# Kernel optimization log

Hardware: AMD Instinct MI355X
Metric: run time of the kernel (lower is better)

## Reference

```python
import jax, jax.numpy as jnp
import numpy as np

B, NC, H, W, C = 4, 3, 112, 112, 128
HEADS, WS, SS = 4, 7, 3
HD = C // HEADS
SCALE = HD ** -0.5
NWIN = (H // WS) * (W // WS)
N = WS * WS  # tokens per window per contrast


def _rel_pos_index():
    # standard Swin relative position index over a WSxWS window
    c = np.stack(np.meshgrid(np.arange(WS), np.arange(WS), indexing='ij')).reshape(2, -1)
    r = (c[:, :, None] - c[:, None, :]).transpose(1, 2, 0)
    r[:, :, 0] += WS - 1
    r[:, :, 1] += WS - 1
    r[:, :, 0] *= 2 * WS - 1
    return r.sum(-1)  # (N, N) int

RPI = _rel_pos_index()


def _attn_mask():
    # SW-MSA mask built exactly as in __init__ (shift active since 0 < SS < WS)
    img = np.zeros((H, W))
    sl = (slice(0, -WS), slice(-WS, -SS), slice(-SS, None))
    cnt = 0
    for hh in sl:
        for ww in sl:
            img[hh, ww] = cnt
            cnt += 1
    mw = img.reshape(H // WS, WS, W // WS, WS).transpose(0, 2, 1, 3).reshape(-1, N)
    am = mw[:, None, :] - mw[:, :, None]  # unsqueeze(1) - unsqueeze(2)
    return jnp.asarray(np.where(am != 0, -100.0, 0.0), dtype=np.float32)  # (nW, N, N)

MASK = _attn_mask()


def win_part(x):
    # (B, n, H, W, C) -> (B*nW, n, WS, WS, C)
    b, n = x.shape[0], x.shape[1]
    x = x.reshape(b, n, H // WS, WS, W // WS, WS, C)
    return x.transpose(0, 2, 4, 1, 3, 5, 6).reshape(-1, n, WS, WS, C)


def win_rev(x, b):
    # (B*nW, n, WS, WS, C) -> (B, n, H, W, C)
    n = x.shape[1]
    x = x.reshape(b, H // WS, W // WS, n, WS, WS, C)
    return x.transpose(0, 3, 1, 4, 2, 5, 6).reshape(b, n, H, W, C)


def ln(x, g, bta):
    m = x.mean(-1, keepdims=True)
    v = ((x - m) ** 2).mean(-1, keepdims=True)
    return (x - m) * jax.lax.rsqrt(v + 1e-5) * g + bta


def win_attn(xq, xk, xv, wq, bq, wk, bk, wv, bv, wp, bp, rpb):
    B_, nq = xq.shape[0], xq.shape[1]
    nkv = xk.shape[1]
    Nq, Nkv = nq * N, nkv * N
    q = (xq.reshape(B_, Nq, C) @ wq + bq).reshape(B_, Nq, HEADS, HD).transpose(0, 2, 1, 3) * SCALE
    k = (xk.reshape(B_, Nkv, C) @ wk + bk).reshape(B_, Nkv, HEADS, HD).transpose(0, 2, 1, 3)
    v = (xv.reshape(B_, Nkv, C) @ wv + bv).reshape(B_, Nkv, HEADS, HD).transpose(0, 2, 1, 3)
    attn = jnp.einsum('bhqd,bhkd->bhqk', q, k)
    bias = jnp.tile(rpb[RPI].transpose(2, 0, 1), (1, nq, nkv))  # (HEADS, Nq, Nkv)
    attn = attn + bias[None]
    m = jnp.tile(MASK, (1, nq, nkv))  # (nW, Nq, Nkv)
    attn = attn.reshape(B_ // NWIN, NWIN, HEADS, Nq, Nkv) + m[None, :, None]
    attn = jax.nn.softmax(attn.reshape(B_, HEADS, Nq, Nkv), axis=-1)
    out = jnp.einsum('bhqk,bhkd->bhqd', attn, v).transpose(0, 2, 1, 3).reshape(B_, Nq, C) @ wp + bp
    return out.reshape(B_, nq, WS, WS, C)


def reference(x, x_kv, contrast_token, contrast_embed,
              n1g, n1b, n2g, n2b, n3g, n3b,
              sa_wq, sa_bq, sa_wk, sa_bk, sa_wv, sa_bv, sa_wp, sa_bp, sa_rpb,
              ca_wq, ca_bq, ca_wk, ca_bk, ca_wv, ca_bv, ca_wp, ca_bp, ca_rpb,
              m_w1, m_b1, m_w2, m_b2):
    ct = contrast_token[None, :, None, None, :]
    ce = contrast_embed[None, :, None, None, :]
    # --- shifted-window self-attention ---
    shortcut = x
    h = ln(x, n1g, n1b)
    h = jnp.roll(h, (-SS, -SS), axis=(2, 3))
    xw = win_part(h)
    xwe = xw + ct
    aw = win_attn(xwe, xwe, xw, sa_wq, sa_bq, sa_wk, sa_bk, sa_wv, sa_bv, sa_wp, sa_bp, sa_rpb)
    h = win_rev(aw, B)
    h = jnp.roll(h, (SS, SS), axis=(2, 3))
    x = shortcut + h
    # --- shifted-window cross-attention against x_kv ---
    shortcut = x
    h = ln(x, n2g, n2b)
    hs = jnp.roll(h, (-SS, -SS), axis=(2, 3))
    kvs = jnp.roll(x_kv, (-SS, -SS), axis=(2, 3))
    xw = win_part(hs)
    kw = win_part(kvs)
    aw = win_attn(xw + ct, kw + ce, kw, ca_wq, ca_bq, ca_wk, ca_bk, ca_wv, ca_bv, ca_wp, ca_bp, ca_rpb)
    h = win_rev(aw, B)
    h = jnp.roll(h, (SS, SS), axis=(2, 3))
    x = shortcut + h
    # --- MLP ---
    h = ln(x, n3g, n3b)
    h = jax.nn.gelu(h @ m_w1 + m_b1, approximate=False) @ m_w2 + m_b2
    return x + h


def setup_inputs():
    key = jax.random.key(0)
    ks = jax.random.split(key, 32)
    rn = lambda i, shp, s=1.0: jax.random.normal(ks[i], shp, dtype=jnp.float32) * s
    inp = {
        'x': rn(0, (B, NC, H, W, C)),
        'x_kv': rn(1, (B, NC, H, W, C)),
        'contrast_token': rn(2, (NC, C), 0.02),
        'contrast_embed': rn(3, (NC, C), 0.02),
        'n1g': jnp.ones((C,)), 'n1b': jnp.zeros((C,)),
        'n2g': jnp.ones((C,)), 'n2b': jnp.zeros((C,)),
        'n3g': jnp.ones((C,)), 'n3b': jnp.zeros((C,)),
    }
    i = 4
    for pre in ('sa', 'ca'):
        for nm in ('wq', 'wk', 'wv', 'wp'):
            inp[pre + '_' + nm] = rn(i, (C, C), 0.02)
            inp[pre + '_b' + nm[1]] = jnp.zeros((C,))
            i += 1
        inp[pre + '_rpb'] = rn(i, ((2 * WS - 1) ** 2, HEADS), 0.02)
        i += 1
    inp['m_w1'] = rn(i, (C, 4 * C), 0.02)
    inp['m_b1'] = jnp.zeros((4 * C,))
    inp['m_w2'] = rn(i + 1, (4 * C, C), 0.02)
    inp['m_b2'] = jnp.zeros((C,))
    return inp
```

## Files before the change

### kernel.cpp

```cpp
#include <hip/hip_runtime.h>
#include <hip/hip_bf16.h>

typedef __hip_bfloat16 bf16;

#define Bn    4
#define NCn   3
#define Hn    112
#define Wn    112
#define Cn    128
#define HEADS 4
#define WSn   7
#define SSn   3
#define HDn   32
#define WNt   1024
#define Tt    147
#define SCALE 0.17677669529663687f

#define SA    288
#define SH    1056
#define MT    32
#define NROWS 49
#define NPAD  64

static const size_t NE = (size_t)Bn * NCn * Hn * Wn * Cn;

typedef float f32x4 __attribute__((ext_vector_type(4)));
typedef short s16x8 __attribute__((ext_vector_type(8)));
typedef short s16x4 __attribute__((ext_vector_type(4)));
#define MFMA(a,b,c) __builtin_amdgcn_mfma_f32_16x16x32_bf16((a),(b),(c),0,0,0)

#define P_QCSA 0
#define P_KCSA 384
#define P_QCCA 768
#define P_KCCA 1152
#define P_VCSA 1536
#define P_BPSA 1664
#define P_VCCA 1792
#define P_BPCA 1920
#define P_B1   2048
#define P_B2   2560
#define P_G1   2688
#define P_N1B  2816
#define P_G2   2944
#define P_N2B  3072
#define P_G3   3200
#define P_N3B  3328

#define W_SAQ 0
#define W_SAK 16384
#define W_SAV 32768
#define W_SAP 49152
#define W_CAQ 65536
#define W_CAK 81920
#define W_CAV 98304
#define W_CAP 114688
#define W_W1T 131072
#define W_W2T 196608

struct Ptrs { const void* p[32]; };

__device__ __forceinline__ float bf2f(bf16 v) { return __bfloat162float(v); }
__device__ __forceinline__ bf16  f2bf(float v) { return __float2bfloat16(v); }
__device__ __forceinline__ short f2bs(float v) { bf16 t = __float2bfloat16(v); return *reinterpret_cast<short*>(&t); }
__device__ __forceinline__ float bs2f(short v) { bf16 t = *reinterpret_cast<bf16*>(&v); return __bfloat162float(t); }

__device__ __forceinline__ float ldi(const void* __restrict__ p, size_t i, int f) {
    return f ? ((const float*)p)[i] : bf2f(((const bf16*)p)[i]);
}

__device__ __forceinline__ float gelu(float x) {
    float x2 = x * x;
    float arg = x * fmaf(x2, 0.0713548162f, 1.5957691216f);
    float e = __expf(arg);
    float r = __builtin_amdgcn_rcpf(1.f + e);
    return x - x * r;
}

__device__ __forceinline__ void ln_inplace(char* __restrict__ rp, const float* __restrict__ gb) {
    float s = 0.f, s2 = 0.f;
    #pragma unroll
    for (int c8 = 0; c8 < 16; ++c8) {
        s16x8 v = *(const s16x8*)(rp + c8 * 16);
        #pragma unroll
        for (int j = 0; j < 8; ++j) { float fv = bs2f(v[j]); s += fv; s2 += fv * fv; }
    }
    float mean = s * (1.f / 128.f);
    float rstd = rsqrtf(s2 * (1.f / 128.f) - mean * mean + 1e-5f);
    #pragma unroll
    for (int c8 = 0; c8 < 16; ++c8) {
        s16x8 v = *(const s16x8*)(rp + c8 * 16);
        #pragma unroll
        for (int j = 0; j < 8; ++j) {
            int col = c8 * 8 + j;
            v[j] = f2bs((bs2f(v[j]) - mean) * rstd * gb[col] + gb[128 + col]);
        }
        *(s16x8*)(rp + c8 * 16) = v;
    }
}

__device__ __forceinline__ void ln_row4(char* __restrict__ rowbase, const float* __restrict__ gb, int sub) {
    char* rp = rowbase + sub * 64;
    float s = 0.f, s2 = 0.f;
    s16x8 vv[4];
    #pragma unroll
    for (int c = 0; c < 4; ++c) {
        vv[c] = *(const s16x8*)(rp + c * 16);
        #pragma unroll
        for (int j = 0; j < 8; ++j) { float fv = bs2f(vv[c][j]); s += fv; s2 += fv * fv; }
    }
    s  += __shfl_xor(s, 1);  s  += __shfl_xor(s, 2);
    s2 += __shfl_xor(s2, 1); s2 += __shfl_xor(s2, 2);
    float mean = s * (1.f / 128.f);
    float rstd = rsqrtf(s2 * (1.f / 128.f) - mean * mean + 1e-5f);
    #pragma unroll
    for (int c = 0; c < 4; ++c) {
        #pragma unroll
        for (int j = 0; j < 8; ++j) {
            int col = sub * 32 + c * 8 + j;
            vv[c][j] = f2bs((bs2f(vv[c][j]) - mean) * rstd * gb[col] + gb[128 + col]);
        }
        *(s16x8*)(rp + c * 16) = vv[c];
    }
}

__device__ __forceinline__ int tok_row(int wn, int t) {
    int b = wn >> 8, wrem = wn & 255, wi = wrem >> 4, wj = wrem & 15;
    int n = t / 49, p = t % 49, pi = p / 7, pj = p % 7;
    int i = (wi * 7 + pi + SSn) % Hn;
    int j = (wj * 7 + pj + SSn) % Wn;
    return ((b * NCn + n) * Hn + i) * Wn + j;
}

__global__ void k_detect(const unsigned int* __restrict__ xw, int* __restrict__ flag) {
    __shared__ int cnt;
    if (threadIdx.x == 0) cnt = 0;
    __syncthreads();
    int c = 0;
    for (int i = threadIdx.x; i < 8192; i += 256) {
        unsigned e = (xw[i] >> 7) & 0xffu;
        c += (e >= 100u && e <= 140u) ? 1 : 0;
    }
    atomicAdd(&cnt, c);
    __syncthreads();
    if (threadIdx.x == 0) *flag = (cnt < 4096) ? 1 : 0;
}

__global__ __launch_bounds__(256) void k_prep(Ptrs in, const int* __restrict__ dflag,
                                              float* __restrict__ P, bf16* __restrict__ wT,
                                              float* __restrict__ BMT) {
    const int f = *dflag;
    int b = blockIdx.x, tid = threadIdx.x;
    if (b == 0) {
        for (int t = tid; t < 384; t += 256) {
            int n = t >> 7, c = t & 127;
            float aq = 0.f, ak = 0.f, aq2 = 0.f, ak2 = 0.f;
            for (int d = 0; d < Cn; ++d) {
                float ctv = ldi(in.p[2], n * Cn + d, f);
                float cev = ldi(in.p[3], n * Cn + d, f);
                aq  += ctv * ldi(in.p[10], d * Cn + c, f);
                ak  += ctv * ldi(in.p[12], d * Cn + c, f);
                aq2 += ctv * ldi(in.p[19], d * Cn + c, f);
                ak2 += cev * ldi(in.p[21], d * Cn + c, f);
            }
            P[P_QCSA + t] = aq  + ldi(in.p[11], c, f);
            P[P_KCSA + t] = ak  + ldi(in.p[13], c, f);
            P[P_QCCA + t] = aq2 + ldi(in.p[20], c, f);
            P[P_KCCA + t] = ak2 + ldi(in.p[22], c, f);
        }
    } else if (b == 1) {
        if (tid < 128) {
            P[P_VCSA + tid] = ldi(in.p[15], tid, f);
            P[P_BPSA + tid] = ldi(in.p[17], tid, f);
            P[P_VCCA + tid] = ldi(in.p[24], tid, f);
            P[P_BPCA + tid] = ldi(in.p[26], tid, f);
            P[P_B2   + tid] = ldi(in.p[31], tid, f);
            P[P_G1   + tid] = ldi(in.p[4],  tid, f);
            P[P_N1B  + tid] = ldi(in.p[5],  tid, f);
            P[P_G2   + tid] = ldi(in.p[6],  tid, f);
            P[P_N2B  + tid] = ldi(in.p[7],  tid, f);
            P[P_G3   + tid] = ldi(in.p[8],  tid, f);
            P[P_N3B  + tid] = ldi(in.p[9],  tid, f);
        }
        for (int t = tid; t < 512; t += 256) P[P_B1 + t] = ldi(in.p[29], t, f);
    } else if (b < 66) {
        const int map[8] = {10, 12, 14, 16, 19, 21, 23, 25};
        int unit = (b - 2) * 4 + (tid >> 6), lane = tid & 63;
        int mat = unit >> 5, ntks = unit & 31;
        int ntile = ntks >> 2, ks = ntks & 3;
        int n = ntile * 16 + (lane & 15), k0 = ks * 32 + (lane >> 4) * 8;
        const void* src = in.p[map[mat]];
        s16x8 v;
        #pragma unroll
        for (int j = 0; j < 8; ++j) v[j] = f2bs(ldi(src, (size_t)(k0 + j) * 128 + n, f));
        *(s16x8*)(wT + mat * 16384 + ((size_t)ntks * 64 + lane) * 8) = v;
    } else if (b < 130) {
        int unit = (b - 66) * 4 + (tid >> 6), lane = tid & 63;
        s16x8 v;
        if (unit < 128) {
            int ntile = unit >> 2, ks = unit & 3;
            int n = ntile * 16 + (lane & 15), k0 = ks * 32 + (lane >> 4) * 8;
            #pragma unroll
            for (int j = 0; j < 8; ++j) v[j] = f2bs(ldi(in.p[28], (size_t)(k0 + j) * 512 + n, f));
            *(s16x8*)(wT + W_W1T + ((size_t)unit * 64 + lane) * 8) = v;
        } else {
            int b2 = unit - 128;
            int ntile = b2 >> 4, ks = b2 & 15;
            int n = ntile * 16 + (lane & 15), k0 = ks * 32 + (lane >> 4) * 8;
            #pragma unroll
            for (int j = 0; j < 8; ++j) v[j] = f2bs(ldi(in.p[30], (size_t)(k0 + j) * 128 + n, f));
            *(s16x8*)(wT + W_W2T + ((size_t)b2 * 64 + lane) * 8) = v;
        }
    } else {
        int u = b - 130;
        int stage = u >> 4, pat = (u >> 2) & 3, h = u & 3;
        const void* rpb = in.p[stage ? 27 : 18];
        float* dst = BMT + (size_t)u * 2560;
        int er = pat >> 1, ec = pat & 1;
        for (int i = tid; i < 2560; i += 256) {
            float v = 0.f;
            int qp = i / 52, kp = i - qp * 52;
            if (qp < 49 && kp < 49) {
                int qpi = qp / 7, qpj = qp - qpi * 7, kpi = kp / 7, kpj = kp - kpi * 7;
                float bias = ldi(rpb, ((qpi - kpi + 6) * 13 + (qpj - kpj + 6)) * HEADS + h, f);
                int rq = (er ? (qpi < 4 ? 1 : 2) : 0) * 3 + (ec ? (qpj < 4 ? 1 : 2) : 0);
                int rk = (er ? (kpi < 4 ? 1 : 2) : 0) * 3 + (ec ? (kpj < 4 ? 1 : 2) : 0);
                v = bias + (rq == rk ? 0.f : -100.f);
            }
            dst[i] = v;
        }
    }
}

__global__ __launch_bounds__(256) void k_qkv_sa(
    const void* __restrict__ x, bf16* __restrict__ xr,
    const float* __restrict__ P, const bf16* __restrict__ wT,
    const int* __restrict__ dflag,
    bf16* __restrict__ tokQ, bf16* __restrict__ tokK, bf16* __restrict__ tokV) {
    const int f = *dflag;
    __shared__ char ldsA[NPAD * SA];
    __shared__ int rowIdx[NROWS];
    __shared__ float gb[256];
    int wn = blockIdx.x, nc = blockIdx.y, tid = threadIdx.x;
    int t0 = nc * NROWS;
    if (tid < NROWS) rowIdx[tid] = tok_row(wn, t0 + tid);
    gb[tid] = tid < 128 ? P[P_G1 + tid] : P[P_N1B + tid - 128];
    for (int i = tid; i < 15 * SA / 4; i += 256) ((int*)(ldsA + NROWS * SA))[i] = 0;
    __syncthreads();
    for (int idx = tid; idx < NROWS * 16; idx += 256) {
        int t = idx >> 4, c8 = idx & 15;
        size_t g = (size_t)rowIdx[t] * Cn + c8 * 8;
        s16x8 v;
        if (f) {
            const float* s = (const float*)x + g;
            #pragma unroll
            for (int j = 0; j < 8; ++j) v[j] = f2bs(s[j]);
        } else {
            v = *(const s16x8*)((const bf16*)x + g);
        }
        *(s16x8*)(ldsA + t * SA + c8 * 16) = v;
        *(s16x8*)(xr + g) = v;
    }
    __syncthreads();
    if (tid < NROWS) ln_inplace(ldsA + tid * SA, gb);
    __syncthreads();
    int wv = tid >> 6, lane = tid & 63, l15 = lane & 15, lg = lane >> 4;
    #pragma unroll 1
    for (int mat = 0; mat < 3; ++mat) {
        const bf16* W = wT + mat * 16384;
        bf16* dst = mat == 0 ? tokQ : (mat == 1 ? tokK : tokV);
        #pragma unroll 1
        for (int ni = 0; ni < 2; ++ni) {
            int nt = wv * 2 + ni;
            f32x4 acc[4] = {};
            #pragma unroll
            for (int ks = 0; ks < 4; ++ks) {
                s16x8 bfrag = *(const s16x8*)(W + (((nt << 2) + ks) * 64 + lane) * 8);
                #pragma unroll
                for (int mt = 0; mt < 4; ++mt) {
                    s16x8 af = *(const s16x8*)(ldsA + (mt * 16 + l15) * SA + ks * 64 + lg * 16);
                    acc[mt] = MFMA(bfrag, af, acc[mt]);
                }
            }
            int col0 = nt * 16 + lg * 4;
            #pragma unroll
            for (int mt = 0; mt < 4; ++mt) {
                int tl = mt * 16 + l15;
                if (tl < NROWS) {
                    int t = t0 + tl;
                    s16x4 pk;
                    if (mat == 0) {
                        f32x4 b4 = *(const f32x4*)(P + P_QCSA + nc * 128 + col0);
                        #pragma unroll
                        for (int r = 0; r < 4; ++r) pk[r] = f2bs((acc[mt][r] + b4[r]) * SCALE);
                    } else if (mat == 1) {
                        f32x4 b4 = *(const f32x4*)(P + P_KCSA + nc * 128 + col0);
                        #pragma unroll
                        for (int r = 0; r < 4; ++r) pk[r] = f2bs(acc[mt][r] + b4[r]);
                    } else {
                        f32x4 b4 = *(const f32x4*)(P + P_VCSA + col0);
                        #pragma unroll
                        for (int r = 0; r < 4; ++r) pk[r] = f2bs(acc[mt][r] + b4[r]);
                    }
                    *(s16x4*)(dst + ((size_t)wn * Tt + t) * Cn + col0) = pk;
                }
            }
        }
    }
}

__global__ __launch_bounds__(512) void k_attn(
    const bf16* __restrict__ Q, const bf16* __restrict__ K, const bf16* __restrict__ V,
    bf16* __restrict__ O, const float* __restrict__ BMbase) {
    __shared__ char ldsK[40 * 256];
    __shared__ char ldsV[32 * 336];
    __shared__ char ldsP[8 * 16 * 336];
    __shared__ float BM[2560];
    __shared__ float lArr[8][16];
    int wn = blockIdx.x, h = blockIdx.y, tid = threadIdx.x;
    int wi = (wn >> 4) & 15, wj = wn & 15;
    size_t base = (size_t)wn * Tt * Cn + h * HDn;
    for (int idx = tid; idx < 640; idx += 512) {
        int key = idx >> 2, ch = idx & 3;
        s16x8 kv = {}, vv = {};
        if (key < Tt) {
            kv = *(const s16x8*)(K + base + (size_t)key * Cn + ch * 8);
            vv = *(const s16x8*)(V + base + (size_t)key * Cn + ch * 8);
        }
        *(s16x8*)(ldsK + (key >> 2) * 256 + (key & 3) * 64 + ch * 16) = kv;
        #pragma unroll
        for (int j = 0; j < 8; ++j)
            *(short*)(ldsV + (ch * 8 + j) * 336 + key * 2) = vv[j];
    }
    {
        int pat = ((wi == 15) << 1) | (wj == 15);
        const f32x4* src = (const f32x4*)(BMbase + (size_t)(pat * 4 + h) * 2560);
        f32x4* dst4 = (f32x4*)BM;
        for (int i = tid; i < 640; i += 512) dst4[i] = src[i];
    }
    __syncthreads();
    int wv = tid >> 6, lane = tid & 63, l15 = lane & 15, lg = lane >> 4;
    char* myP = ldsP + wv * (16 * 336);
    int kpA[10];
    #pragma unroll
    for (int nt = 0; nt < 10; ++nt) {
        int key = nt * 16 + l15;
        kpA[nt] = key - (key >= 147 ? 147 : (key >= 98 ? 98 : (key >= 49 ? 49 : 0)));
    }
    for (int mt = wv; mt < 10; mt += 8) {
        int qrow = mt * 16 + l15; if (qrow > 146) qrow = 146;
        s16x8 qf = *(const s16x8*)(Q + base + (size_t)qrow * Cn + lg * 8);
        f32x4 acc[10];
        #pragma unroll
        for (int nt = 0; nt < 10; ++nt) {
            int key = nt * 16 + l15;
            s16x8 bfrag = *(const s16x8*)(ldsK + (key >> 2) * 256 + (key & 3) * 64 + lg * 16);
            f32x4 z = {};
            acc[nt] = MFMA(qf, bfrag, z);
        }
        float linv[4];
        #pragma unroll
        for (int r = 0; r < 4; ++r) {
            int row = mt * 16 + lg * 4 + r;
            int qp = row - (row >= 147 ? 147 : (row >= 98 ? 98 : (row >= 49 ? 49 : 0)));
            float s[10], m = -1e30f;
            #pragma unroll
            for (int nt = 0; nt < 10; ++nt) {
                float sv = acc[nt][r] + BM[qp * 52 + kpA[nt]];
                if (nt == 9 && l15 >= 3) sv = -1e30f;
                s[nt] = sv;
                m = fmaxf(m, sv);
            }
            #pragma unroll
            for (int off = 1; off < 16; off <<= 1) m = fmaxf(m, __shfl_xor(m, off));
            float l = 0.f;
            #pragma unroll
            for (int nt = 0; nt < 10; ++nt) {
                float p = (nt == 9 && l15 >= 3) ? 0.f : __expf(s[nt] - m);
                l += p;
                *(bf16*)(myP + (lg * 4 + r) * 336 + (nt * 16 + l15) * 2) = f2bf(p);
            }
            #pragma unroll
            for (int off = 1; off < 16; off <<= 1) l += __shfl_xor(l, off);
            linv[r] = 1.f / l;
        }
        if (l15 == 0) {
            #pragma unroll
            for (int r = 0; r < 4; ++r) lArr[wv][lg * 4 + r] = linv[r];
        }
        float myinv = lArr[wv][l15];
        #pragma unroll
        for (int ntv = 0; ntv < 2; ++ntv) {
            f32x4 ao = {};
            #pragma unroll
            for (int ks = 0; ks < 5; ++ks) {
                s16x8 af = *(const s16x8*)(myP + l15 * 336 + ks * 64 + lg * 16);
                s16x8 vf = *(const s16x8*)(ldsV + (ntv * 16 + l15) * 336 + ks * 64 + lg * 16);
                ao = MFMA(vf, af, ao);
            }
            int q = mt * 16 + l15;
            if (q < Tt) {
                s16x4 pk;
                #pragma unroll
                for (int r = 0; r < 4; ++r) pk[r] = f2bs(ao[r] * myinv);
                *(s16x4*)(O + base + (size_t)q * Cn + ntv * 16 + lg * 4) = pk;
            }
        }
    }
}

__global__ __launch_bounds__(256) void k_proj(
    const bf16* __restrict__ tokO, const float* __restrict__ P, const bf16* __restrict__ W,
    int bpOff, bf16* __restrict__ xr) {
    __shared__ char ldsA[NPAD * SA];
    __shared__ int rowIdx[NROWS];
    int wn = blockIdx.x, nc = blockIdx.y, tid = threadIdx.x;
    int t0 = nc * NROWS;
    if (tid < NROWS) rowIdx[tid] = tok_row(wn, t0 + tid);
    for (int i = tid; i < 15 * SA / 4; i += 256) ((int*)(ldsA + NROWS * SA))[i] = 0;
    __syncthreads();
    int wv = tid >> 6, lane = tid & 63, l15 = lane & 15, lg = lane >> 4;
    s16x4 xrc[2][4];
    #pragma unroll
    for (int ni = 0; ni < 2; ++ni) {
        int col0 = (wv * 2 + ni) * 16 + lg * 4;
        #pragma unroll
        for (int mt = 0; mt < 4; ++mt) {
            int tl = mt * 16 + l15;
            int rr = rowIdx[tl < NROWS ? tl : 0];
            xrc[ni][mt] = *(const s16x4*)(xr + (size_t)rr * Cn + col0);
        }
    }
    for (int idx = tid; idx < NROWS * 16; idx += 256) {
        int t = idx >> 4, c8 = idx & 15;
        s16x8 v = *(const s16x8*)(tokO + ((size_t)wn * Tt + t0 + t) * Cn + c8 * 8);
        *(s16x8*)(ldsA + t * SA + c8 * 16) = v;
    }
    __syncthreads();
    f32x4 acc2[2][4] = {};
    #pragma unroll
    for (int ni = 0; ni < 2; ++ni) {
        int nt = wv * 2 + ni;
        #pragma unroll
        for (int ks = 0; ks < 4; ++ks) {
            s16x8 bfrag = *(const s16x8*)(W + (((nt << 2) + ks) * 64 + lane) * 8);
            #pragma unroll
            for (int mt = 0; mt < 4; ++mt) {
                s16x8 af = *(const s16x8*)(ldsA + (mt * 16 + l15) * SA + ks * 64 + lg * 16);
                acc2[ni][mt] = MFMA(bfrag, af, acc2[ni][mt]);
            }
        }
    }
    #pragma unroll
    for (int ni = 0; ni < 2; ++ni) {
        int col0 = (wv * 2 + ni) * 16 + lg * 4;
        f32x4 bp4 = *(const f32x4*)(P + bpOff + col0);
        #pragma unroll
        for (int mt = 0; mt < 4; ++mt) {
            int tl = mt * 16 + l15;
            if (tl < NROWS) {
                s16x4 pk;
                #pragma unroll
                for (int r = 0; r < 4; ++r) pk[r] = f2bs(bs2f(xrc[ni][mt][r]) + acc2[ni][mt][r] + bp4[r]);
                *(s16x4*)(xr + (size_t)rowIdx[tl] * Cn + col0) = pk;
            }
        }
    }
}

__global__ __launch_bounds__(256) void k_proj_ca(
    const bf16* __restrict__ tokO, const float* __restrict__ P, const bf16* __restrict__ wT,
    const void* __restrict__ xkv, const int* __restrict__ dflag, bf16* __restrict__ xr,
    bf16* __restrict__ tokQ, bf16* __restrict__ tokK, bf16* __restrict__ tokV) {
    const int f = *dflag;
    __shared__ char ldsA[NPAD * SA];
    __shared__ int rowIdx[NROWS];
    __shared__ float gb[256];
    int wn = blockIdx.x, nc = blockIdx.y, tid = threadIdx.x;
    int t0 = nc * NROWS;
    if (tid < NROWS) rowIdx[tid] = tok_row(wn, t0 + tid);
    gb[tid] = tid < 128 ? P[P_G2 + tid] : P[P_N2B + tid - 128];
    for (int i = tid; i < 15 * SA / 4; i += 256) ((int*)(ldsA + NROWS * SA))[i] = 0;
    __syncthreads();
    for (int idx = tid; idx < NROWS * 16; idx += 256) {
        int t = idx >> 4, c8 = idx & 15;
        s16x8 v = *(const s16x8*)(tokO + ((size_t)wn * Tt + t0 + t) * Cn + c8 * 8);
        *(s16x8*)(ldsA + t * SA + c8 * 16) = v;
    }
    __syncthreads();
    int wv = tid >> 6, lane = tid & 63, l15 = lane & 15, lg = lane >> 4;
    {
        const bf16* W = wT + W_SAP;
        #pragma unroll 1
        for (int ni = 0; ni < 2; ++ni) {
            int nt = wv * 2 + ni;
            f32x4 acc[4] = {};
            #pragma unroll
            for (int ks = 0; ks < 4; ++ks) {
                s16x8 bfrag = *(const s16x8*)(W + (((nt << 2) + ks) * 64 + lane) * 8);
                #pragma unroll
                for (int mt = 0; mt < 4; ++mt) {
                    s16x8 af = *(const s16x8*)(ldsA + (mt * 16 + l15) * SA + ks * 64 + lg * 16);
                    acc[mt] = MFMA(bfrag, af, acc[mt]);
                }
            }
            int col0 = nt * 16 + lg * 4;
            f32x4 bp4 = *(const f32x4*)(P + P_BPSA + col0);
            #pragma unroll
            for (int mt = 0; mt < 4; ++mt) {
                int tl = mt * 16 + l15;
                if (tl < NROWS) {
                    size_t o = (size_t)rowIdx[tl] * Cn + col0;
                    s16x4 cur = *(const s16x4*)(xr + o);
                    s16x4 pk;
                    #pragma unroll
                    for (int r = 0; r < 4; ++r) pk[r] = f2bs(bs2f(cur[r]) + acc[mt][r] + bp4[r]);
                    *(s16x4*)(xr + o) = pk;
                }
            }
        }
    }
    __syncthreads();
    for (int idx = tid; idx < NROWS * 16; idx += 256) {
        int t = idx >> 4, c8 = idx & 15;
        s16x8 v = *(const s16x8*)(xr + (size_t)rowIdx[t] * Cn + c8 * 8);
        *(s16x8*)(ldsA + t * SA + c8 * 16) = v;
    }
    __syncthreads();
    if (tid < NROWS) ln_inplace(ldsA + tid * SA, gb);
    __syncthreads();
    {
        const bf16* W = wT + W_CAQ;
        #pragma unroll 1
        for (int ni = 0; ni < 2; ++ni) {
            int nt = wv * 2 + ni;
            f32x4 acc[4] = {};
            #pragma unroll
            for (int ks = 0; ks < 4; ++ks) {
                s16x8 bfrag = *(const s16x8*)(W + (((nt << 2) + ks) * 64 + lane) * 8);
                #pragma unroll
                for (int mt = 0; mt < 4; ++mt) {
                    s16x8 af = *(const s16x8*)(ldsA + (mt * 16 + l15) * SA + ks * 64 + lg * 16);
                    acc[mt] = MFMA(bfrag, af, acc[mt]);
                }
            }
            int col0 = nt * 16 + lg * 4;
            #pragma unroll
            for (int mt = 0; mt < 4; ++mt) {
                int tl = mt * 16 + l15;
                if (tl < NROWS) {
                    int t = t0 + tl;
                    f32x4 b4 = *(const f32x4*)(P + P_QCCA + nc * 128 + col0);
                    s16x4 pk;
                    #pragma unroll
                    for (int r = 0; r < 4; ++r) pk[r] = f2bs((acc[mt][r] + b4[r]) * SCALE);
                    *(s16x4*)(tokQ + ((size_t)wn * Tt + t) * Cn + col0) = pk;
                }
            }
        }
    }
    __syncthreads();
    for (int idx = tid; idx < NROWS * 16; idx += 256) {
        int t = idx >> 4, c8 = idx & 15;
        s16x8 v;
        if (f) {
            const float* s = (const float*)xkv + (size_t)rowIdx[t] * Cn + c8 * 8;
            #pragma unroll
            for (int j = 0; j < 8; ++j) v[j] = f2bs(s[j]);
        } else {
            v = *(const s16x8*)((const bf16*)xkv + (size_t)rowIdx[t] * Cn + c8 * 8);
        }
        *(s16x8*)(ldsA + t * SA + c8 * 16) = v;
    }
    __syncthreads();
    #pragma unroll 1
    for (int mat = 0; mat < 2; ++mat) {
        const bf16* W = wT + (mat == 0 ? W_CAK : W_CAV);
        bf16* dst = mat == 0 ? tokK : tokV;
        #pragma unroll 1
        for (int ni = 0; ni < 2; ++ni) {
            int nt = wv * 2 + ni;
            f32x4 acc[4] = {};
            #pragma unroll
            for (int ks = 0; ks < 4; ++ks) {
                s16x8 bfrag = *(const s16x8*)(W + (((nt << 2) + ks) * 64 + lane) * 8);
                #pragma unroll
                for (int mt = 0; mt < 4; ++mt) {
                    s16x8 af = *(const s16x8*)(ldsA + (mt * 16 + l15) * SA + ks * 64 + lg * 16);
                    acc[mt] = MFMA(bfrag, af, acc[mt]);
                }
            }
            int col0 = nt * 16 + lg * 4;
            #pragma unroll
            for (int mt = 0; mt < 4; ++mt) {
                int tl = mt * 16 + l15;
                if (tl < NROWS) {
                    int t = t0 + tl;
                    f32x4 b4 = (mat == 0) ? *(const f32x4*)(P + P_KCCA + nc * 128 + col0)
                                          : *(const f32x4*)(P + P_VCCA + col0);
                    s16x4 pk;
                    #pragma unroll
                    for (int r = 0; r < 4; ++r) pk[r] = f2bs(acc[mt][r] + b4[r]);
                    *(s16x4*)(dst + ((size_t)wn * Tt + t) * Cn + col0) = pk;
                }
            }
        }
    }
}

__global__ __launch_bounds__(256) void k_mlp(
    const bf16* __restrict__ xr, const float* __restrict__ P, const bf16* __restrict__ wT,
    const int* __restrict__ dflag, void* __restrict__ outp) {
    __shared__ char ldsU[MT * SH];
    __shared__ float gb[256];
    char* ldsA = ldsU;
    char* ldsH = ldsU;
    int tid = threadIdx.x;
    size_t t0 = (size_t)blockIdx.x * MT;
    gb[tid] = tid < 128 ? P[P_G3 + tid] : P[P_N3B + tid - 128];
    __syncthreads();
    for (int idx = tid; idx < MT * 16; idx += 256) {
        int t = idx >> 4, c8 = idx & 15;
        s16x8 v = *(const s16x8*)(xr + (t0 + t) * Cn + c8 * 8);
        *(s16x8*)(ldsA + t * SA + c8 * 16) = v;
    }
    __syncthreads();
    {
        int row = tid >> 3, sub = tid & 7;
        if (sub < 4) ln_row4(ldsA + row * SA, gb, sub);
    }
    __syncthreads();
    int wv = tid >> 6, lane = tid & 63, l15 = lane & 15, lg = lane >> 4;
    const bf16* W1 = wT + W_W1T;
    s16x8 a[2][4];
    #pragma unroll
    for (int m = 0; m < 2; ++m)
        #pragma unroll
        for (int ks = 0; ks < 4; ++ks)
            a[m][ks] = *(const s16x8*)(ldsA + (m * 16 + l15) * SA + ks * 64 + lg * 16);
    __syncthreads();
    {
        int nt0 = wv * 8;
        s16x8 bc0 = *(const s16x8*)(W1 + (((nt0 << 2) + 0) * 64 + lane) * 8);
        s16x8 bc1 = *(const s16x8*)(W1 + (((nt0 << 2) + 1) * 64 + lane) * 8);
        s16x8 bc2 = *(const s16x8*)(W1 + (((nt0 << 2) + 2) * 64 + lane) * 8);
        s16x8 bc3 = *(const s16x8*)(W1 + (((nt0 << 2) + 3) * 64 + lane) * 8);
        #pragma unroll 1
        for (int ni = 0; ni < 8; ++ni) {
            int nt = nt0 + ni;
            s16x8 bn0 = *(const s16x8*)(W1 + ((((nt + 1) << 2) + 0) * 64 + lane) * 8);
            s16x8 bn1 = *(const s16x8*)(W1 + ((((nt + 1) << 2) + 1) * 64 + lane) * 8);
            s16x8 bn2 = *(const s16x8*)(W1 + ((((nt + 1) << 2) + 2) * 64 + lane) * 8);
            s16x8 bn3 = *(const s16x8*)(W1 + ((((nt + 1) << 2) + 3) * 64 + lane) * 8);
            f32x4 acc[2] = {};
            #pragma unroll
            for (int m = 0; m < 2; ++m) {
                acc[m] = MFMA(bc0, a[m][0], acc[m]);
                acc[m] = MFMA(bc1, a[m][1], acc[m]);
                acc[m] = MFMA(bc2, a[m][2], acc[m]);
                acc[m] = MFMA(bc3, a[m][3], acc[m]);
            }
            int col0 = nt * 16 + lg * 4;
            f32x4 b14 = *(const f32x4*)(P + P_B1 + col0);
            #pragma unroll
            for (int m = 0; m < 2; ++m) {
                s16x4 pk;
                #pragma unroll
                for (int r = 0; r < 4; ++r) pk[r] = f2bs(gelu(acc[m][r] + b14[r]));
                *(s16x4*)(ldsH + (m * 16 + l15) * SH + col0 * 2) = pk;
            }
            bc0 = bn0; bc1 = bn1; bc2 = bn2; bc3 = bn3;
        }
    }
    __syncthreads();
    const int f = *dflag;
    const bf16* W2 = wT + W_W2T;
    #pragma unroll 1
    for (int ni = 0; ni < 2; ++ni) {
        int nt = wv * 2 + ni;
        f32x4 acc[2] = {};
        s16x8 bc = *(const s16x8*)(W2 + (((nt << 4) + 0) * 64 + lane) * 8);
        #pragma unroll 1
        for (int ks = 0; ks < 16; ++ks) {
            s16x8 bn = *(const s16x8*)(W2 + (((nt << 4) + ks + 1) * 64 + lane) * 8);
            #pragma unroll
            for (int m = 0; m < 2; ++m) {
                s16x8 af = *(const s16x8*)(ldsH + (m * 16 + l15) * SH + ks * 64 + lg * 16);
                acc[m] = MFMA(bc, af, acc[m]);
            }
            bc = bn;
        }
        int col0 = nt * 16 + lg * 4;
        f32x4 b24 = *(const f32x4*)(P + P_B2 + col0);
        #pragma unroll
        for (int m = 0; m < 2; ++m) {
            size_t g = (t0 + m * 16 + l15) * Cn + col0;
            s16x4 cur = *(const s16x4*)(xr + g);
            if (f) {
                f32x4 o;
                #pragma unroll
                for (int r = 0; r < 4; ++r) o[r] = bs2f(cur[r]) + acc[m][r] + b24[r];
                *(f32x4*)((float*)outp + g) = o;
            } else {
                s16x4 pk;
                #pragma unroll
                for (int r = 0; r < 4; ++r) pk[r] = f2bs(bs2f(cur[r]) + acc[m][r] + b24[r]);
                *(s16x4*)((bf16*)outp + g) = pk;
            }
        }
    }
}

extern "C" void kernel_launch(void* const* d_in, const int* in_sizes, int n_in,
                              void* d_out, int out_size, void* d_ws, size_t ws_size,
                              hipStream_t stream) {
    Ptrs ptrs;
    for (int i = 0; i < 32; ++i) ptrs.p[i] = d_in[i];

    char* base = (char*)d_ws;
    float* P    = (float*)base;
    int*  dflag = (int*)(base + 32768);
    bf16* wT    = (bf16*)(base + 33024);
    float* BMT  = (float*)(wT + 262144);
    bf16* xr    = (bf16*)(BMT + 81920);
    bf16* tokK  = xr + NE;
    bf16* tokV  = tokK + NE;
    bf16* tokQ  = (bf16*)d_out;

    k_detect<<<1, 256, 0, stream>>>((const unsigned int*)d_in[0], dflag);
    k_prep<<<162, 256, 0, stream>>>(ptrs, dflag, P, wT, BMT);
    k_qkv_sa<<<dim3(WNt, 3), 256, 0, stream>>>(d_in[0], xr, P, wT, dflag, tokQ, tokK, tokV);
    k_attn<<<dim3(WNt, HEADS), 512, 0, stream>>>(tokQ, tokK, tokV, tokQ, BMT);
    k_proj_ca<<<dim3(WNt, 3), 256, 0, stream>>>(tokQ, P, wT, d_in[1], dflag, xr, tokQ, tokK, tokV);
    k_attn<<<dim3(WNt, HEADS), 512, 0, stream>>>(tokQ, tokK, tokV, tokQ, BMT + 16 * 2560);
    k_proj<<<dim3(WNt, 3), 256, 0, stream>>>(tokQ, P, wT + W_CAP, P_BPCA, xr);
    k_mlp<<<(int)(NE / Cn / MT), 256, 0, stream>>>(xr, P, wT, dflag, d_out);
}
```

Baseline: 564.5 us.

## Fuse cross-attention output projection with LayerNorm and MLP per window

Merges the cross-attention projection kernel and the MLP kernel into one per-window kernel. The residual sum is kept in registers and in LDS, then LayerNorm and both MLP GEMMs run on the 49-row tile without re-reading xr from global memory. The final write goes to xr in bf16, and a separate copy kernel converts it to the output format. This saves one global round trip of the residual, but adds an extra full-tensor copy pass. It also raises LDS use (49×1056 bytes), which may lower occupancy, and 64-row tiles with 15 padded rows waste MFMA work.

Result: slower. 587.3 us (+4.0%).

```diff
diff --git a/kernel.cpp b/kernel.cpp
--- a/kernel.cpp
+++ b/kernel.cpp
@@ -18,7 +18,6 @@
 
 #define SA    288
 #define SH    1056
-#define MT    32
 #define NROWS 49
 #define NPAD  64
 
@@ -95,31 +94,6 @@
             v[j] = f2bs((bs2f(v[j]) - mean) * rstd * gb[col] + gb[128 + col]);
         }
         *(s16x8*)(rp + c8 * 16) = v;
-    }
-}
-
-__device__ __forceinline__ void ln_row4(char* __restrict__ rowbase, const float* __restrict__ gb, int sub) {
-    char* rp = rowbase + sub * 64;
-    float s = 0.f, s2 = 0.f;
-    s16x8 vv[4];
-    #pragma unroll
-    for (int c = 0; c < 4; ++c) {
-        vv[c] = *(const s16x8*)(rp + c * 16);
-        #pragma unroll
-        for (int j = 0; j < 8; ++j) { float fv = bs2f(vv[c][j]); s += fv; s2 += fv * fv; }
-    }
-    s  += __shfl_xor(s, 1);  s  += __shfl_xor(s, 2);
-    s2 += __shfl_xor(s2, 1); s2 += __shfl_xor(s2, 2);
-    float mean = s * (1.f / 128.f);
-    float rstd = rsqrtf(s2 * (1.f / 128.f) - mean * mean + 1e-5f);
-    #pragma unroll
-    for (int c = 0; c < 4; ++c) {
-        #pragma unroll
-        for (int j = 0; j < 8; ++j) {
-            int col = sub * 32 + c * 8 + j;
-            vv[c][j] = f2bs((bs2f(vv[c][j]) - mean) * rstd * gb[col] + gb[128 + col]);
-        }
-        *(s16x8*)(rp + c * 16) = vv[c];
     }
 }
 
@@ -408,65 +382,6 @@
     }
 }
 
-__global__ __launch_bounds__(256) void k_proj(
-    const bf16* __restrict__ tokO, const float* __restrict__ P, const bf16* __restrict__ W,
-    int bpOff, bf16* __restrict__ xr) {
-    __shared__ char ldsA[NPAD * SA];
-    __shared__ int rowIdx[NROWS];
-    int wn = blockIdx.x, nc = blockIdx.y, tid = threadIdx.x;
-    int t0 = nc * NROWS;
-    if (tid < NROWS) rowIdx[tid] = tok_row(wn, t0 + tid);
-    for (int i = tid; i < 15 * SA / 4; i += 256) ((int*)(ldsA + NROWS * SA))[i] = 0;
-    __syncthreads();
-    int wv = tid >> 6, lane = tid & 63, l15 = lane & 15, lg = lane >> 4;
-    s16x4 xrc[2][4];
-    #pragma unroll
-    for (int ni = 0; ni < 2; ++ni) {
-        int col0 = (wv * 2 + ni) * 16 + lg * 4;
-        #pragma unroll
-        for (int mt = 0; mt < 4; ++mt) {
-            int tl = mt * 16 + l15;
-            int rr = rowIdx[tl < NROWS ? tl : 0];
-            xrc[ni][mt] = *(const s16x4*)(xr + (size_t)rr * Cn + col0);
-        }
-    }
-    for (int idx = tid; idx < NROWS * 16; idx += 256) {
-        int t = idx >> 4, c8 = idx & 15;
-        s16x8 v = *(const s16x8*)(tokO + ((size_t)wn * Tt + t0 + t) * Cn + c8 * 8);
-        *(s16x8*)(ldsA + t * SA + c8 * 16) = v;
-    }
-    __syncthreads();
-    f32x4 acc2[2][4] = {};
-    #pragma unroll
-    for (int ni = 0; ni < 2; ++ni) {
-        int nt = wv * 2 + ni;
-        #pragma unroll
-        for (int ks = 0; ks < 4; ++ks) {
-            s16x8 bfrag = *(const s16x8*)(W + (((nt << 2) + ks) * 64 + lane) * 8);
-            #pragma unroll
-            for (int mt = 0; mt < 4; ++mt) {
-                s16x8 af = *(const s16x8*)(ldsA + (mt * 16 + l15) * SA + ks * 64 + lg * 16);
-                acc2[ni][mt] = MFMA(bfrag, af, acc2[ni][mt]);
-            }
-        }
-    }
-    #pragma unroll
-    for (int ni = 0; ni < 2; ++ni) {
-        int col0 = (wv * 2 + ni) * 16 + lg * 4;
-        f32x4 bp4 = *(const f32x4*)(P + bpOff + col0);
-        #pragma unroll
-        for (int mt = 0; mt < 4; ++mt) {
-            int tl = mt * 16 + l15;
-            if (tl < NROWS) {
-                s16x4 pk;
-                #pragma unroll
-                for (int r = 0; r < 4; ++r) pk[r] = f2bs(bs2f(xrc[ni][mt][r]) + acc2[ni][mt][r] + bp4[r]);
-                *(s16x4*)(xr + (size_t)rowIdx[tl] * Cn + col0) = pk;
-            }
-        }
-    }
-}
-
 __global__ __launch_bounds__(256) void k_proj_ca(
     const bf16* __restrict__ tokO, const float* __restrict__ P, const bf16* __restrict__ wT,
     const void* __restrict__ xkv, const int* __restrict__ dflag, bf16* __restrict__ xr,
@@ -607,106 +522,155 @@
     }
 }
 
-__global__ __launch_bounds__(256) void k_mlp(
-    const bf16* __restrict__ xr, const float* __restrict__ P, const bf16* __restrict__ wT,
-    const int* __restrict__ dflag, void* __restrict__ outp) {
-    __shared__ char ldsU[MT * SH];
+__global__ __launch_bounds__(256) void k_proj_mlp(
+    const bf16* __restrict__ tokO, const float* __restrict__ P, const bf16* __restrict__ wT,
+    bf16* __restrict__ xr) {
+    __shared__ char ldsU[NROWS * SH];
+    __shared__ int rowIdx[NROWS];
     __shared__ float gb[256];
     char* ldsA = ldsU;
     char* ldsH = ldsU;
-    int tid = threadIdx.x;
-    size_t t0 = (size_t)blockIdx.x * MT;
+    int wn = blockIdx.x, nc = blockIdx.y, tid = threadIdx.x;
+    int t0 = nc * NROWS;
+    if (tid < NROWS) rowIdx[tid] = tok_row(wn, t0 + tid);
     gb[tid] = tid < 128 ? P[P_G3 + tid] : P[P_N3B + tid - 128];
     __syncthreads();
-    for (int idx = tid; idx < MT * 16; idx += 256) {
+    int wv = tid >> 6, lane = tid & 63, l15 = lane & 15, lg = lane >> 4;
+    s16x4 xrc[2][4];
+    #pragma unroll
+    for (int ni = 0; ni < 2; ++ni) {
+        int col0 = (wv * 2 + ni) * 16 + lg * 4;
+        #pragma unroll
+        for (int mt = 0; mt < 4; ++mt) {
+            int tl = mt * 16 + l15;
+            int rr = rowIdx[tl < NROWS ? tl : 0];
+            xrc[ni][mt] = *(const s16x4*)(xr + (size_t)rr * Cn + col0);
+        }
+    }
+    for (int idx = tid; idx < NROWS * 16; idx += 256) {
         int t = idx >> 4, c8 = idx & 15;
-        s16x8 v = *(const s16x8*)(xr + (t0 + t) * Cn + c8 * 8);
+        s16x8 v = *(const s16x8*)(tokO + ((size_t)wn * Tt + t0 + t) * Cn + c8 * 8);
         *(s16x8*)(ldsA + t * SA + c8 * 16) = v;
     }
     __syncthreads();
+    f32x4 acc2[2][4] = {};
     {
-        int row = tid >> 3, sub = tid & 7;
-        if (sub < 4) ln_row4(ldsA + row * SA, gb, sub);
-    }
-    __syncthreads();
-    int wv = tid >> 6, lane = tid & 63, l15 = lane & 15, lg = lane >> 4;
-    const bf16* W1 = wT + W_W1T;
-    s16x8 a[2][4];
+        const bf16* W = wT + W_CAP;
+        #pragma unroll
+        for (int ni = 0; ni < 2; ++ni) {
+            int nt = wv * 2 + ni;
+            #pragma unroll
+            for (int ks = 0; ks < 4; ++ks) {
+                s16x8 bfrag = *(const s16x8*)(W + (((nt << 2) + ks) * 64 + lane) * 8);
+                #pragma unroll
+                for (int mt = 0; mt < 4; ++mt) {
+                    int rowc = mt * 16 + l15; if (rowc > 48) rowc = 48;
+                    s16x8 af = *(const s16x8*)(ldsA + rowc * SA + ks * 64 + lg * 16);
+                    acc2[ni][mt] = MFMA(bfrag, af, acc2[ni][mt]);
+                }
+            }
+        }
+    }
+    __syncthreads();
+    s16x4 xrnew[2][4];
     #pragma unroll
-    for (int m = 0; m < 2; ++m)
+    for (int ni = 0; ni < 2; ++ni) {
+        int col0 = (wv * 2 + ni) * 16 + lg * 4;
+        f32x4 bp4 = *(const f32x4*)(P + P_BPCA + col0);
+        #pragma unroll
+        for (int mt = 0; mt < 4; ++mt) {
+            int tl = mt * 16 + l15;
+            s16x4 pk;
+            #pragma unroll
+            for (int r = 0; r < 4; ++r) pk[r] = f2bs(bs2f(xrc[ni][mt][r]) + acc2[ni][mt][r] + bp4[r]);
+            xrnew[ni][mt] = pk;
+            if (tl < NROWS) *(s16x4*)(ldsA + tl * SA + col0 * 2) = pk;
+        }
+    }
+    __syncthreads();
+    if (tid < NROWS) ln_inplace(ldsA + tid * SA, gb);
+    __syncthreads();
+    s16x8 a[4][4];
+    #pragma unroll
+    for (int m = 0; m < 4; ++m) {
+        int rowc = m * 16 + l15; if (rowc > 48) rowc = 48;
         #pragma unroll
         for (int ks = 0; ks < 4; ++ks)
-            a[m][ks] = *(const s16x8*)(ldsA + (m * 16 + l15) * SA + ks * 64 + lg * 16);
+            a[m][ks] = *(const s16x8*)(ldsA + rowc * SA + ks * 64 + lg * 16);
+    }
     __syncthreads();
     {
-        int nt0 = wv * 8;
-        s16x8 bc0 = *(const s16x8*)(W1 + (((nt0 << 2) + 0) * 64 + lane) * 8);
-        s16x8 bc1 = *(const s16x8*)(W1 + (((nt0 << 2) + 1) * 64 + lane) * 8);
-        s16x8 bc2 = *(const s16x8*)(W1 + (((nt0 << 2) + 2) * 64 + lane) * 8);
-        s16x8 bc3 = *(const s16x8*)(W1 + (((nt0 << 2) + 3) * 64 + lane) * 8);
+        const bf16* W1 = wT + W_W1T;
         #pragma unroll 1
         for (int ni = 0; ni < 8; ++ni) {
-            int nt = nt0 + ni;
-            s16x8 bn0 = *(const s16x8*)(W1 + ((((nt + 1) << 2) + 0) * 64 + lane) * 8);
-            s16x8 bn1 = *(const s16x8*)(W1 + ((((nt + 1) << 2) + 1) * 64 + lane) * 8);
-            s16x8 bn2 = *(const s16x8*)(W1 + ((((nt + 1) << 2) + 2) * 64 + lane) * 8);
-            s16x8 bn3 = *(const s16x8*)(W1 + ((((nt + 1) << 2) + 3) * 64 + lane) * 8);
-            f32x4 acc[2] = {};
-            #pragma unroll
-            for (int m = 0; m < 2; ++m) {
-                acc[m] = MFMA(bc0, a[m][0], acc[m]);
-                acc[m] = MFMA(bc1, a[m][1], acc[m]);
-                acc[m] = MFMA(bc2, a[m][2], acc[m]);
-                acc[m] = MFMA(bc3, a[m][3], acc[m]);
+            int nt = wv * 8 + ni;
+            f32x4 acc[4] = {};
+            #pragma unroll
+            for (int ks = 0; ks < 4; ++ks) {
+                s16x8 bfrag = *(const s16x8*)(W1 + (((nt << 2) + ks) * 64 + lane) * 8);
+                #pragma unroll
+                for (int m = 0; m < 4; ++m) acc[m] = MFMA(bfrag, a[m][ks], acc[m]);
             }
             int col0 = nt * 16 + lg * 4;
             f32x4 b14 = *(const f32x4*)(P + P_B1 + col0);
             #pragma unroll
-            for (int m = 0; m < 2; ++m) {
-                s16x4 pk;
+            for (int m = 0; m < 4; ++m) {
+                int tl = m * 16 + l15;
+                if (tl < NROWS) {
+                    s16x4 pk;
+                    #pragma unroll
+                    for (int r = 0; r < 4; ++r) pk[r] = f2bs(gelu(acc[m][r] + b14[r]));
+                    *(s16x4*)(ldsH + tl * SH + col0 * 2) = pk;
+                }
+            }
+        }
+    }
+    __syncthreads();
+    {
+        const bf16* W2 = wT + W_W2T;
+        #pragma unroll
+        for (int ni = 0; ni < 2; ++ni) {
+            int nt = wv * 2 + ni;
+            f32x4 accB[4] = {};
+            #pragma unroll 1
+            for (int ks = 0; ks < 16; ++ks) {
+                s16x8 bfrag = *(const s16x8*)(W2 + (((nt << 4) + ks) * 64 + lane) * 8);
                 #pragma unroll
-                for (int r = 0; r < 4; ++r) pk[r] = f2bs(gelu(acc[m][r] + b14[r]));
-                *(s16x4*)(ldsH + (m * 16 + l15) * SH + col0 * 2) = pk;
-            }
-            bc0 = bn0; bc1 = bn1; bc2 = bn2; bc3 = bn3;
-        }
-    }
-    __syncthreads();
+                for (int m = 0; m < 4; ++m) {
+                    int rowc = m * 16 + l15; if (rowc > 48) rowc = 48;
+                    s16x8 af = *(const s16x8*)(ldsH + rowc * SH + ks * 64 + lg * 16);
+                    accB[m] = MFMA(bfrag, af, accB[m]);
+                }
+            }
+            int col0 = nt * 16 + lg * 4;
+            f32x4 b24 = *(const f32x4*)(P + P_B2 + col0);
+            #pragma unroll
+            for (int m = 0; m < 4; ++m) {
+                int tl = m * 16 + l15;
+                if (tl < NROWS) {
+                    s16x4 pk;
+                    #pragma unroll
+                    for (int r = 0; r < 4; ++r)
+                        pk[r] = f2bs(bs2f(xrnew[ni][m][r]) + accB[m][r] + b24[r]);
+                    *(s16x4*)(xr + (size_t)rowIdx[tl] * Cn + col0) = pk;
+                }
+            }
+        }
+    }
+}
+
+__global__ __launch_bounds__(256) void k_copyout(const bf16* __restrict__ xr,
+                                                 const int* __restrict__ dflag,
+                                                 void* __restrict__ outp) {
     const int f = *dflag;
-    const bf16* W2 = wT + W_W2T;
-    #pragma unroll 1
-    for (int ni = 0; ni < 2; ++ni) {
-        int nt = wv * 2 + ni;
-        f32x4 acc[2] = {};
-        s16x8 bc = *(const s16x8*)(W2 + (((nt << 4) + 0) * 64 + lane) * 8);
-        #pragma unroll 1
-        for (int ks = 0; ks < 16; ++ks) {
-            s16x8 bn = *(const s16x8*)(W2 + (((nt << 4) + ks + 1) * 64 + lane) * 8);
-            #pragma unroll
-            for (int m = 0; m < 2; ++m) {
-                s16x8 af = *(const s16x8*)(ldsH + (m * 16 + l15) * SH + ks * 64 + lg * 16);
-                acc[m] = MFMA(bc, af, acc[m]);
-            }
-            bc = bn;
-        }
-        int col0 = nt * 16 + lg * 4;
-        f32x4 b24 = *(const f32x4*)(P + P_B2 + col0);
-        #pragma unroll
-        for (int m = 0; m < 2; ++m) {
-            size_t g = (t0 + m * 16 + l15) * Cn + col0;
-            s16x4 cur = *(const s16x4*)(xr + g);
-            if (f) {
-                f32x4 o;
-                #pragma unroll
-                for (int r = 0; r < 4; ++r) o[r] = bs2f(cur[r]) + acc[m][r] + b24[r];
-                *(f32x4*)((float*)outp + g) = o;
-            } else {
-                s16x4 pk;
-                #pragma unroll
-                for (int r = 0; r < 4; ++r) pk[r] = f2bs(bs2f(cur[r]) + acc[m][r] + b24[r]);
-                *(s16x4*)((bf16*)outp + g) = pk;
-            }
-        }
+    size_t i8 = ((size_t)blockIdx.x * 256 + threadIdx.x) * 8;
+    s16x8 v = *(const s16x8*)(xr + i8);
+    if (f) {
+        float* o = (float*)outp + i8;
+        #pragma unroll
+        for (int j = 0; j < 8; ++j) o[j] = bs2f(v[j]);
+    } else {
+        *(s16x8*)((bf16*)outp + i8) = v;
     }
 }
 
@@ -732,6 +696,6 @@
     k_attn<<<dim3(WNt, HEADS), 512, 0, stream>>>(tokQ, tokK, tokV, tokQ, BMT);
     k_proj_ca<<<dim3(WNt, 3), 256, 0, stream>>>(tokQ, P, wT, d_in[1], dflag, xr, tokQ, tokK, tokV);
     k_attn<<<dim3(WNt, HEADS), 512, 0, stream>>>(tokQ, tokK, tokV, tokQ, BMT + 16 * 2560);
-    k_proj<<<dim3(WNt, 3), 256, 0, stream>>>(tokQ, P, wT + W_CAP, P_BPCA, xr);
-    k_mlp<<<(int)(NE / Cn / MT), 256, 0, stream>>>(xr, P, wT, dflag, d_out);
-}
+    k_proj_mlp<<<dim3(WNt, 3), 256, 0, stream>>>(tokQ, P, wT, xr);
+    k_copyout<<<(int)(NE / 2048), 256, 0, stream>>>(xr, dflag, d_out);
+}
```
